# Performance work log

Measured on AMD Instinct MI355X. Metric: run time of the kernel, lower is better.

Reference implementation:

```python
import jax, jax.numpy as jnp
import numpy as np

N = 40000       # nodes
DEG = 16        # in-degree per node (self-constructed so in_deg > 0)
E = N * DEG     # edges
DIN = 128       # in_ent_feats == out_ent_feats
H = 8           # num_heads
D = DIN // H    # head_dim = 16
FF = 4 * DIN    # FFN hidden
HOPS = 5
ALPHA = 0.15
EPS = 1e-5


def _ln(x, g, b):
    m = jnp.mean(x, axis=-1, keepdims=True)
    v = jnp.mean((x - m) ** 2, axis=-1, keepdims=True)
    return (x - m) / jnp.sqrt(v + EPS) * g + b


def setup_inputs() -> dict:
    key = jax.random.key(0)
    ks = jax.random.split(key, 12)
    s = 0.05
    feat = jax.random.normal(ks[0], (N, DIN), dtype=jnp.float32)
    src = jax.random.randint(ks[1], (E,), 0, N, dtype=jnp.int32)
    # every node gets exactly DEG incoming edges -> in_degree > 0 everywhere
    dst = jnp.repeat(jnp.arange(N, dtype=jnp.int32), DEG)
    return {
        "feat": feat,
        "Wh": jax.random.normal(ks[2], (DIN, DIN), dtype=jnp.float32) * s,
        "Wt": jax.random.normal(ks[3], (DIN, DIN), dtype=jnp.float32) * s,
        "We": jax.random.normal(ks[4], (DIN, DIN), dtype=jnp.float32) * s,
        "attn_p": jax.random.normal(ks[5], (H, D), dtype=jnp.float32) * s,
        "g_head": jax.random.normal(ks[6], (H, D), dtype=jnp.float32) * s,
        "g_tail": jax.random.normal(ks[7], (H, D), dtype=jnp.float32) * s,
        "ln1_g": jnp.ones((DIN,), jnp.float32),
        "ln1_b": jnp.zeros((DIN,), jnp.float32),
        "ln2_g": jnp.ones((DIN,), jnp.float32),
        "ln2_b": jnp.zeros((DIN,), jnp.float32),
        "W1": jax.random.normal(ks[8], (FF, DIN), dtype=jnp.float32) * s,
        "b1": jnp.zeros((FF,), jnp.float32),
        "W2": jax.random.normal(ks[9], (DIN, FF), dtype=jnp.float32) * s,
        "b2": jnp.zeros((DIN,), jnp.float32),
        "src": src,
        "dst": dst,
    }


def reference(feat, Wh, Wt, We, attn_p, g_head, g_tail, ln1_g, ln1_b,
              ln2_g, ln2_b, W1, b1, W2, b2, src, dst):
    n = feat.shape[0]
    h = _ln(feat, ln1_g, ln1_b)                      # feat_drop is identity (eval)
    fh = (h @ Wh.T).reshape(n, H, D)                 # feat_head
    ft = (h @ Wt.T).reshape(n, H, D)                 # feat_tail
    fe = (h @ We.T).reshape(n, H, D)                 # feat_enti ('ft' in dgl)

    # attention logits: (u_mul_v . attn).sum(-1) / head_dim, scaled by log(in_deg) of dst
    e = jnp.sum(fh[src] * ft[dst] * attn_p, axis=-1) / D          # [E, H]
    in_deg = jax.ops.segment_sum(jnp.ones_like(dst, jnp.float32), dst, num_segments=n)
    log_in = jnp.log(in_deg)                                       # [N]
    e = e * log_in[dst][:, None]

    # gate scores
    gh = jnp.sum(fh * g_head, axis=-1)                             # [N, H]
    gt = jnp.sum(ft * g_tail, axis=-1)
    gate = jax.nn.sigmoid(gh[src] + gt[dst])                       # [E, H]

    # weighted edge softmax (per-dst stabilized, gated)
    mx = jax.ops.segment_max(e, dst, num_segments=n)               # [N, H]
    tag = jnp.exp(e - mx[dst]) * gate
    ssum = jax.ops.segment_sum(tag, dst, num_segments=n)
    a = tag / ssum[dst]                                            # [E, H]

    # PPR diffusion
    feat0 = fe
    f = feat0
    for _ in range(HOPS):
        msg = f[src] * a[..., None]                                # [E, H, D]
        agg = jax.ops.segment_sum(msg, dst, num_segments=n)
        f = (1.0 - ALPHA) * agg + ALPHA * feat0

    # residual (Identity since in == out), flatten, FFN block
    rst = (f + feat.reshape(n, H, D)).reshape(n, -1)               # [N, DIN]
    x = _ln(rst, ln2_g, ln2_b)
    ff = jax.nn.relu(x @ W1.T + b1) @ W2.T + b2
    return ff + rst
```

## Files before the change

kernel.cpp:

```cpp
#include <hip/hip_runtime.h>
#include <math.h>

#define N_NODES 40000
#define DEG 16
#define DIN 128
#define NH 8
#define DH 16
#define FFDIM 512
#define ALPHA 0.15f
#define LNEPS 1e-5f

typedef __attribute__((ext_vector_type(8))) short bf16x8;
typedef __attribute__((ext_vector_type(4))) float f32x4;
typedef __attribute__((ext_vector_type(4))) unsigned int u32x4;

__device__ inline unsigned int f2bf(float f) {
    unsigned int u = __float_as_uint(f);
    return (u + 0x7fffu + ((u >> 16) & 1u)) >> 16;
}
__device__ inline float bflo(unsigned u) { return __uint_as_float(u << 16); }
__device__ inline float bfhi(unsigned u) { return __uint_as_float(u & 0xffff0000u); }

__device__ inline float dot8(u32x4 uf, u32x4 ut, const float* __restrict__ ap) {
    float s = 0.f;
#pragma unroll
    for (int k = 0; k < 4; ++k) {
        s += bflo(uf[k]) * bflo(ut[k]) * ap[2 * k]
           + bfhi(uf[k]) * bfhi(ut[k]) * ap[2 * k + 1];
    }
    return s;
}

__device__ inline float wave_sum64(float v) {
#pragma unroll
    for (int m = 32; m >= 1; m >>= 1) v += __shfl_xor(v, m, 64);
    return v;
}

__global__ void cvt_weights(const float* __restrict__ wh, const float* __restrict__ wt,
                            const float* __restrict__ we, const float* __restrict__ w1,
                            const float* __restrict__ w2,
                            short* __restrict__ owh, short* __restrict__ owt,
                            short* __restrict__ owe, short* __restrict__ ow1,
                            short* __restrict__ ow2) {
    int i = blockIdx.x * 256 + threadIdx.x;
    if (i < 16384)       owh[i]          = (short)f2bf(wh[i]);
    else if (i < 32768)  owt[i - 16384]  = (short)f2bf(wt[i - 16384]);
    else if (i < 49152)  owe[i - 32768]  = (short)f2bf(we[i - 32768]);
    else if (i < 114688) ow1[i - 49152]  = (short)f2bf(w1[i - 49152]);
    else if (i < 180224) ow2[i - 114688] = (short)f2bf(w2[i - 114688]);
}

__global__ void ln_kernel(const float* __restrict__ in, const float* __restrict__ g,
                          const float* __restrict__ b, short* __restrict__ out, int n) {
    int wid  = (blockIdx.x * blockDim.x + threadIdx.x) >> 6;
    int lane = threadIdx.x & 63;
    if (wid >= n) return;
    float2 v = *(const float2*)(in + (size_t)wid * DIN + lane * 2);
    float mean = wave_sum64(v.x + v.y) * (1.0f / DIN);
    float dx = v.x - mean, dy = v.y - mean;
    float var = wave_sum64(dx * dx + dy * dy) * (1.0f / DIN);
    float rstd = rsqrtf(var + LNEPS);
    float2 gg = *(const float2*)(g + lane * 2);
    float2 bb = *(const float2*)(b + lane * 2);
    float o0 = dx * rstd * gg.x + bb.x, o1 = dy * rstd * gg.y + bb.y;
    unsigned int pack = f2bf(o0) | (f2bf(o1) << 16);
    *(unsigned int*)(out + (size_t)wid * DIN + lane * 2) = pack;
}

__global__ void add_ln_kernel(const float* __restrict__ f, const float* __restrict__ feat,
                              const float* __restrict__ g, const float* __restrict__ b,
                              float* __restrict__ rst, short* __restrict__ x, int n) {
    int wid  = (blockIdx.x * blockDim.x + threadIdx.x) >> 6;
    int lane = threadIdx.x & 63;
    if (wid >= n) return;
    float2 va = *(const float2*)(f + (size_t)wid * DIN + lane * 2);
    float2 vb = *(const float2*)(feat + (size_t)wid * DIN + lane * 2);
    float2 r = { va.x + vb.x, va.y + vb.y };
    *(float2*)(rst + (size_t)wid * DIN + lane * 2) = r;
    float mean = wave_sum64(r.x + r.y) * (1.0f / DIN);
    float dx = r.x - mean, dy = r.y - mean;
    float var = wave_sum64(dx * dx + dy * dy) * (1.0f / DIN);
    float rstd = rsqrtf(var + LNEPS);
    float2 gg = *(const float2*)(g + lane * 2);
    float2 bb = *(const float2*)(b + lane * 2);
    float o0 = dx * rstd * gg.x + bb.x, o1 = dy * rstd * gg.y + bb.y;
    unsigned int pack = f2bf(o0) | (f2bf(o1) << 16);
    *(unsigned int*)(x + (size_t)wid * DIN + lane * 2) = pack;
}

__global__ __launch_bounds__(256) void mfma_gemm(
        const short* __restrict__ A, const short* __restrict__ B,
        int M, int N, int K,
        const float* __restrict__ bias, const float* __restrict__ res, int relu,
        float* __restrict__ Cf, short* __restrict__ Cb) {
    __shared__ __align__(16) short Al[64 * 64];
    __shared__ __align__(16) short Bl[128 * 64];
    const int t  = threadIdx.x;
    const int bm = blockIdx.x * 64;
    const int bn = blockIdx.y * 128;
    const int w = t >> 6, lane = t & 63;
    const int wr = w >> 1, wc = w & 1;
    const int l15 = lane & 15, l4 = lane >> 4;
    f32x4 acc[2][4] = {};
    for (int k0 = 0; k0 < K; k0 += 64) {
        __syncthreads();
#pragma unroll
        for (int q = 0; q < 2; ++q) {
            int c = t + q * 256;
            int r = c >> 3, kb = c & 7;
            bf16x8 v = *(const bf16x8*)(A + (size_t)(bm + r) * K + k0 + kb * 8);
            *(bf16x8*)(Al + (r * 8 + (kb ^ (r & 7))) * 8) = v;
        }
#pragma unroll
        for (int q = 0; q < 4; ++q) {
            int c = t + q * 256;
            int r = c >> 3, kb = c & 7;
            bf16x8 v = *(const bf16x8*)(B + (size_t)(bn + r) * K + k0 + kb * 8);
            *(bf16x8*)(Bl + (r * 8 + (kb ^ (r & 7))) * 8) = v;
        }
        __syncthreads();
#pragma unroll
        for (int kc = 0; kc < 2; ++kc) {
            bf16x8 af[2], bfr[4];
#pragma unroll
            for (int mf = 0; mf < 2; ++mf) {
                int row = wr * 32 + mf * 16 + l15;
                int kb = kc * 4 + l4;
                af[mf] = *(const bf16x8*)(Al + (row * 8 + (kb ^ (row & 7))) * 8);
            }
#pragma unroll
            for (int nf = 0; nf < 4; ++nf) {
                int row = wc * 64 + nf * 16 + l15;
                int kb = kc * 4 + l4;
                bfr[nf] = *(const bf16x8*)(Bl + (row * 8 + (kb ^ (row & 7))) * 8);
            }
#pragma unroll
            for (int mf = 0; mf < 2; ++mf)
#pragma unroll
                for (int nf = 0; nf < 4; ++nf)
                    acc[mf][nf] = __builtin_amdgcn_mfma_f32_16x16x32_bf16(
                        af[mf], bfr[nf], acc[mf][nf], 0, 0, 0);
        }
    }
#pragma unroll
    for (int mf = 0; mf < 2; ++mf) {
#pragma unroll
        for (int nf = 0; nf < 4; ++nf) {
            int gcol = bn + wc * 64 + nf * 16 + l15;
            float bv = bias ? bias[gcol] : 0.f;
#pragma unroll
            for (int r = 0; r < 4; ++r) {
                int grow = bm + wr * 32 + mf * 16 + l4 * 4 + r;
                float v = acc[mf][nf][r] + bv;
                if (relu) v = fmaxf(v, 0.f);
                size_t off = (size_t)grow * N + gcol;
                if (res) v += res[off];
                if (Cb) Cb[off] = (short)f2bf(v);
                if (Cf) Cf[off] = v;
            }
        }
    }
}

__global__ void gates_kernel(const short* __restrict__ fh, const short* __restrict__ ftl,
                             const float* __restrict__ g_head, const float* __restrict__ g_tail,
                             float* __restrict__ gh, float* __restrict__ gt, int total) {
    int t = blockIdx.x * blockDim.x + threadIdx.x;
    if (t >= total) return;
    int i = t >> 3, h = t & 7;
    const short* fp = fh + (size_t)i * DIN + h * DH;
    const short* fq = ftl + (size_t)i * DIN + h * DH;
    const float* gp = g_head + h * DH;
    const float* gq = g_tail + h * DH;
    float s1 = 0.f, s2 = 0.f;
#pragma unroll
    for (int d = 0; d < DH; d += 2) {
        unsigned a = *(const unsigned*)(fp + d);
        unsigned b = *(const unsigned*)(fq + d);
        s1 += bflo(a) * gp[d] + bfhi(a) * gp[d + 1];
        s2 += bflo(b) * gq[d] + bfhi(b) * gq[d + 1];
    }
    gh[t] = s1;
    gt[t] = s2;
}

__global__ void attn_kernel(const short* __restrict__ fh, const short* __restrict__ ftl,
                            const float* __restrict__ ghv, const float* __restrict__ gtv,
                            const float* __restrict__ attn_p, const int* __restrict__ src,
                            float* __restrict__ av, int n) {
    int wid  = (blockIdx.x * blockDim.x + threadIdx.x) >> 6;
    int lane = threadIdx.x & 63;
    if (wid >= n) return;
    int e  = lane & 15;
    int h0 = lane >> 4;
    int s = src[(size_t)wid * DEG + e];
    const short* fr0 = fh  + (size_t)s   * DIN + h0 * DH;
    const short* tr0 = ftl + (size_t)wid * DIN + h0 * DH;
    u32x4 f0a = *(const u32x4*)(fr0);
    u32x4 f0b = *(const u32x4*)(fr0 + 8);
    u32x4 t0a = *(const u32x4*)(tr0);
    u32x4 t0b = *(const u32x4*)(tr0 + 8);
    u32x4 f1a = *(const u32x4*)(fr0 + 64);
    u32x4 f1b = *(const u32x4*)(fr0 + 72);
    u32x4 t1a = *(const u32x4*)(tr0 + 64);
    u32x4 t1b = *(const u32x4*)(tr0 + 72);
    const float* ap0 = attn_p + h0 * DH;
    float v0 = dot8(f0a, t0a, ap0) + dot8(f0b, t0b, ap0 + 8);
    float v1 = dot8(f1a, t1a, ap0 + 64) + dot8(f1b, t1b, ap0 + 72);
    const float c = 0.17328679513998632f;
    v0 *= c; v1 *= c;
    float m0 = v0, m1 = v1;
#pragma unroll
    for (int msk = 1; msk <= 8; msk <<= 1) {
        m0 = fmaxf(m0, __shfl_xor(m0, msk, 64));
        m1 = fmaxf(m1, __shfl_xor(m1, msk, 64));
    }
    float gate0 = 1.f / (1.f + expf(-(ghv[(size_t)s * NH + h0]     + gtv[(size_t)wid * NH + h0])));
    float gate1 = 1.f / (1.f + expf(-(ghv[(size_t)s * NH + h0 + 4] + gtv[(size_t)wid * NH + h0 + 4])));
    float t0 = expf(v0 - m0) * gate0;
    float t1 = expf(v1 - m1) * gate1;
    float s0 = t0, s1 = t1;
#pragma unroll
    for (int msk = 1; msk <= 8; msk <<= 1) {
        s0 += __shfl_xor(s0, msk, 64);
        s1 += __shfl_xor(s1, msk, 64);
    }
    float* ao = av + ((size_t)wid * DEG + e) * NH;
    ao[h0]     = t0 / s0;
    ao[h0 + 4] = t1 / s1;
}

__global__ __launch_bounds__(256) void hop_kernel(
        const short* __restrict__ fin, const float* __restrict__ fe,
        const float* __restrict__ av, const int* __restrict__ src,
        short* __restrict__ fout_b, float* __restrict__ fout_f, int n) {
    __shared__ int sidx[4 * DEG];
    int wv   = threadIdx.x >> 6;
    int lane = threadIdx.x & 63;
    int wid  = blockIdx.x * 4 + wv;
    if (threadIdx.x < 4 * DEG) {
        int node = blockIdx.x * 4 + (threadIdx.x >> 4);
        sidx[threadIdx.x] = (node < n) ? src[(size_t)node * DEG + (threadIdx.x & 15)] : 0;
    }
    __syncthreads();
    if (wid >= n) return;
    int grp = lane >> 4;
    int dl  = lane & 15;
    int h   = dl >> 1;
    const float* ae = av + (size_t)wid * (DEG * NH);
    float acc[8] = {};
#pragma unroll
    for (int it = 0; it < 4; ++it) {
        int e = it * 4 + grp;
        int s = sidx[wv * DEG + e];
        float w = ae[e * NH + h];
        u32x4 v = *(const u32x4*)(fin + (size_t)s * DIN + dl * 8);
#pragma unroll
        for (int k = 0; k < 4; ++k) {
            acc[2 * k]     += w * bflo(v[k]);
            acc[2 * k + 1] += w * bfhi(v[k]);
        }
    }
#pragma unroll
    for (int k = 0; k < 8; ++k) {
        acc[k] += __shfl_xor(acc[k], 16, 64);
        acc[k] += __shfl_xor(acc[k], 32, 64);
    }
    if (grp == 0) {
        const float* fp = fe + (size_t)wid * DIN + dl * 8;
        float o[8];
#pragma unroll
        for (int k = 0; k < 8; ++k)
            o[k] = (1.f - ALPHA) * acc[k] + ALPHA * fp[k];
        if (fout_b) {
            unsigned pk[4];
#pragma unroll
            for (int k = 0; k < 4; ++k)
                pk[k] = f2bf(o[2 * k]) | (f2bf(o[2 * k + 1]) << 16);
            *(u32x4*)(fout_b + (size_t)wid * DIN + dl * 8) = *(u32x4*)pk;
        } else {
            float4 a = { o[0], o[1], o[2], o[3] };
            float4 b = { o[4], o[5], o[6], o[7] };
            *(float4*)(fout_f + (size_t)wid * DIN + dl * 8)     = a;
            *(float4*)(fout_f + (size_t)wid * DIN + dl * 8 + 4) = b;
        }
    }
}

extern "C" void kernel_launch(void* const* d_in, const int* in_sizes, int n_in,
                              void* d_out, int out_size, void* d_ws, size_t ws_size,
                              hipStream_t stream) {
    const float* feat   = (const float*)d_in[0];
    const float* Wh     = (const float*)d_in[1];
    const float* Wt     = (const float*)d_in[2];
    const float* We     = (const float*)d_in[3];
    const float* attn_p = (const float*)d_in[4];
    const float* g_head = (const float*)d_in[5];
    const float* g_tail = (const float*)d_in[6];
    const float* ln1_g  = (const float*)d_in[7];
    const float* ln1_b  = (const float*)d_in[8];
    const float* ln2_g  = (const float*)d_in[9];
    const float* ln2_b  = (const float*)d_in[10];
    const float* W1     = (const float*)d_in[11];
    const float* b1     = (const float*)d_in[12];
    const float* W2     = (const float*)d_in[13];
    const float* b2     = (const float*)d_in[14];
    const int*   src    = (const int*)d_in[15];

    float* ws = (float*)d_ws;
    float* fe   = ws;
    float* av   = ws + 5120000;
    float* gh   = ws + 10240000;
    float* gt   = ws + 10560000;
    short* h_bf   = (short*)(ws + 10880000);
    short* fh_bf  = (short*)(ws + 13440000);
    short* ftl_bf = (short*)(ws + 16000000);
    short* fe_bf  = (short*)(ws + 18560000);
    short* f0_bf  = (short*)(ws + 21120000);
    short* f1_bf  = (short*)(ws + 23680000);
    float* ffin   = ws + 26240000;
    short* x_bf   = (short*)(ws + 31360000);
    short* hidden = (short*)ws;
    short* wb     = (short*)(ws + 33920000);
    short* wh_bf = wb, *wt_bf = wb + 16384, *we_bf = wb + 32768;
    short* w1_bf = wb + 49152, *w2_bf = wb + 114688;
    float* rst = (float*)d_out;

    dim3 b256(256);
    int nodeBlocks  = (N_NODES * 64) / 256;
    int nodeBlocks4 = (N_NODES + 3) / 4;

    cvt_weights<<<704, b256, 0, stream>>>(Wh, Wt, We, W1, W2, wh_bf, wt_bf, we_bf, w1_bf, w2_bf);
    ln_kernel<<<nodeBlocks, b256, 0, stream>>>(feat, ln1_g, ln1_b, h_bf, N_NODES);

    dim3 gp(N_NODES / 64, 1);
    mfma_gemm<<<gp, b256, 0, stream>>>(h_bf, wh_bf, N_NODES, DIN, DIN, nullptr, nullptr, 0, nullptr, fh_bf);
    mfma_gemm<<<gp, b256, 0, stream>>>(h_bf, wt_bf, N_NODES, DIN, DIN, nullptr, nullptr, 0, nullptr, ftl_bf);
    mfma_gemm<<<gp, b256, 0, stream>>>(h_bf, we_bf, N_NODES, DIN, DIN, nullptr, nullptr, 0, fe, fe_bf);

    gates_kernel<<<(N_NODES * NH) / 256, b256, 0, stream>>>(fh_bf, ftl_bf, g_head, g_tail, gh, gt, N_NODES * NH);
    attn_kernel<<<nodeBlocks, b256, 0, stream>>>(fh_bf, ftl_bf, gh, gt, attn_p, src, av, N_NODES);

    hop_kernel<<<nodeBlocks4, b256, 0, stream>>>(fe_bf, fe, av, src, f0_bf, nullptr, N_NODES);
    hop_kernel<<<nodeBlocks4, b256, 0, stream>>>(f0_bf, fe, av, src, f1_bf, nullptr, N_NODES);
    hop_kernel<<<nodeBlocks4, b256, 0, stream>>>(f1_bf, fe, av, src, f0_bf, nullptr, N_NODES);
    hop_kernel<<<nodeBlocks4, b256, 0, stream>>>(f0_bf, fe, av, src, f1_bf, nullptr, N_NODES);
    hop_kernel<<<nodeBlocks4, b256, 0, stream>>>(f1_bf, fe, av, src, nullptr, ffin, N_NODES);

    add_ln_kernel<<<nodeBlocks, b256, 0, stream>>>(ffin, feat, ln2_g, ln2_b, rst, x_bf, N_NODES);

    dim3 gff1(N_NODES / 64, FFDIM / 128);
    mfma_gemm<<<gff1, b256, 0, stream>>>(x_bf, w1_bf, N_NODES, FFDIM, DIN, b1, nullptr, 1, nullptr, hidden);
    dim3 gff2(N_NODES / 64, 1);
    mfma_gemm<<<gff2, b256, 0, stream>>>(hidden, w2_bf, N_NODES, DIN, FFDIM, b2, rst, 0, rst, nullptr);
}
```

Before: 367.7 us.

## Store attention weights and feat0 in bf16, stage weights in LDS, enlarge GEMM tile

Attention coefficients are now written as bf16 instead of fp32. The residual feat0 term in each PPR hop is read from the existing bf16 copy, so the fp32 fe buffer is gone. Each hop block loads its nodes' attention weights into shared memory in one coalesced copy. The MFMA GEMM tile grows from 64 to 128 rows per block, with row clamping for the tail. Together these cut memory traffic across the five hop passes and increase reuse in the GEMMs, at the cost of lower precision for attention and feat0, fewer GEMM blocks, and more registers per GEMM thread.

New measurement: 406.8 us. 10.6% more time.

```diff
diff --git a/kernel.cpp b/kernel.cpp
--- a/kernel.cpp
+++ b/kernel.cpp
@@ -20,6 +20,7 @@
 }
 __device__ inline float bflo(unsigned u) { return __uint_as_float(u << 16); }
 __device__ inline float bfhi(unsigned u) { return __uint_as_float(u & 0xffff0000u); }
+__device__ inline float bfs(short s) { return __uint_as_float(((unsigned)(unsigned short)s) << 16); }
 
 __device__ inline float dot8(u32x4 uf, u32x4 ut, const float* __restrict__ ap) {
     float s = 0.f;
@@ -94,38 +95,34 @@
         int M, int N, int K,
         const float* __restrict__ bias, const float* __restrict__ res, int relu,
         float* __restrict__ Cf, short* __restrict__ Cb) {
-    __shared__ __align__(16) short Al[64 * 64];
+    __shared__ __align__(16) short Al[128 * 64];
     __shared__ __align__(16) short Bl[128 * 64];
     const int t  = threadIdx.x;
-    const int bm = blockIdx.x * 64;
+    const int bm = blockIdx.x * 128;
     const int bn = blockIdx.y * 128;
     const int w = t >> 6, lane = t & 63;
     const int wr = w >> 1, wc = w & 1;
     const int l15 = lane & 15, l4 = lane >> 4;
-    f32x4 acc[2][4] = {};
+    f32x4 acc[4][4] = {};
     for (int k0 = 0; k0 < K; k0 += 64) {
         __syncthreads();
-#pragma unroll
-        for (int q = 0; q < 2; ++q) {
-            int c = t + q * 256;
-            int r = c >> 3, kb = c & 7;
-            bf16x8 v = *(const bf16x8*)(A + (size_t)(bm + r) * K + k0 + kb * 8);
-            *(bf16x8*)(Al + (r * 8 + (kb ^ (r & 7))) * 8) = v;
-        }
 #pragma unroll
         for (int q = 0; q < 4; ++q) {
             int c = t + q * 256;
             int r = c >> 3, kb = c & 7;
-            bf16x8 v = *(const bf16x8*)(B + (size_t)(bn + r) * K + k0 + kb * 8);
-            *(bf16x8*)(Bl + (r * 8 + (kb ^ (r & 7))) * 8) = v;
+            int gr = bm + r; if (gr >= M) gr = M - 1;
+            bf16x8 va = *(const bf16x8*)(A + (size_t)gr * K + k0 + kb * 8);
+            *(bf16x8*)(Al + (r * 8 + (kb ^ (r & 7))) * 8) = va;
+            bf16x8 vb = *(const bf16x8*)(B + (size_t)(bn + r) * K + k0 + kb * 8);
+            *(bf16x8*)(Bl + (r * 8 + (kb ^ (r & 7))) * 8) = vb;
         }
         __syncthreads();
 #pragma unroll
         for (int kc = 0; kc < 2; ++kc) {
-            bf16x8 af[2], bfr[4];
-#pragma unroll
-            for (int mf = 0; mf < 2; ++mf) {
-                int row = wr * 32 + mf * 16 + l15;
+            bf16x8 af[4], bfr[4];
+#pragma unroll
+            for (int mf = 0; mf < 4; ++mf) {
+                int row = wr * 64 + mf * 16 + l15;
                 int kb = kc * 4 + l4;
                 af[mf] = *(const bf16x8*)(Al + (row * 8 + (kb ^ (row & 7))) * 8);
             }
@@ -136,7 +133,7 @@
                 bfr[nf] = *(const bf16x8*)(Bl + (row * 8 + (kb ^ (row & 7))) * 8);
             }
 #pragma unroll
-            for (int mf = 0; mf < 2; ++mf)
+            for (int mf = 0; mf < 4; ++mf)
 #pragma unroll
                 for (int nf = 0; nf < 4; ++nf)
                     acc[mf][nf] = __builtin_amdgcn_mfma_f32_16x16x32_bf16(
@@ -144,14 +141,15 @@
         }
     }
 #pragma unroll
-    for (int mf = 0; mf < 2; ++mf) {
+    for (int mf = 0; mf < 4; ++mf) {
 #pragma unroll
         for (int nf = 0; nf < 4; ++nf) {
             int gcol = bn + wc * 64 + nf * 16 + l15;
             float bv = bias ? bias[gcol] : 0.f;
 #pragma unroll
             for (int r = 0; r < 4; ++r) {
-                int grow = bm + wr * 32 + mf * 16 + l4 * 4 + r;
+                int grow = bm + wr * 64 + mf * 16 + l4 * 4 + r;
+                if (grow >= M) continue;
                 float v = acc[mf][nf][r] + bv;
                 if (relu) v = fmaxf(v, 0.f);
                 size_t off = (size_t)grow * N + gcol;
@@ -188,7 +186,7 @@
 __global__ void attn_kernel(const short* __restrict__ fh, const short* __restrict__ ftl,
                             const float* __restrict__ ghv, const float* __restrict__ gtv,
                             const float* __restrict__ attn_p, const int* __restrict__ src,
-                            float* __restrict__ av, int n) {
+                            short* __restrict__ av, int n) {
     int wid  = (blockIdx.x * blockDim.x + threadIdx.x) >> 6;
     int lane = threadIdx.x & 63;
     if (wid >= n) return;
@@ -226,35 +224,38 @@
         s0 += __shfl_xor(s0, msk, 64);
         s1 += __shfl_xor(s1, msk, 64);
     }
-    float* ao = av + ((size_t)wid * DEG + e) * NH;
-    ao[h0]     = t0 / s0;
-    ao[h0 + 4] = t1 / s1;
+    short* ao = av + ((size_t)wid * DEG + e) * NH;
+    ao[h0]     = (short)f2bf(t0 / s0);
+    ao[h0 + 4] = (short)f2bf(t1 / s1);
 }
 
 __global__ __launch_bounds__(256) void hop_kernel(
-        const short* __restrict__ fin, const float* __restrict__ fe,
-        const float* __restrict__ av, const int* __restrict__ src,
+        const short* __restrict__ fin, const short* __restrict__ febf,
+        const short* __restrict__ avb, const int* __restrict__ src,
         short* __restrict__ fout_b, float* __restrict__ fout_f, int n) {
     __shared__ int sidx[4 * DEG];
+    __shared__ short sav[4 * DEG * NH];
     int wv   = threadIdx.x >> 6;
     int lane = threadIdx.x & 63;
-    int wid  = blockIdx.x * 4 + wv;
+    int base = blockIdx.x * 4;
+    int wid  = base + wv;
     if (threadIdx.x < 4 * DEG) {
-        int node = blockIdx.x * 4 + (threadIdx.x >> 4);
+        int node = base + (threadIdx.x >> 4);
         sidx[threadIdx.x] = (node < n) ? src[(size_t)node * DEG + (threadIdx.x & 15)] : 0;
     }
+    ((unsigned*)sav)[threadIdx.x] = ((const unsigned*)(avb + (size_t)base * DEG * NH))[threadIdx.x];
     __syncthreads();
     if (wid >= n) return;
     int grp = lane >> 4;
     int dl  = lane & 15;
     int h   = dl >> 1;
-    const float* ae = av + (size_t)wid * (DEG * NH);
+    const short* ae = sav + wv * DEG * NH;
     float acc[8] = {};
 #pragma unroll
     for (int it = 0; it < 4; ++it) {
         int e = it * 4 + grp;
         int s = sidx[wv * DEG + e];
-        float w = ae[e * NH + h];
+        float w = bfs(ae[e * NH + h]);
         u32x4 v = *(const u32x4*)(fin + (size_t)s * DIN + dl * 8);
 #pragma unroll
         for (int k = 0; k < 4; ++k) {
@@ -268,11 +269,13 @@
         acc[k] += __shfl_xor(acc[k], 32, 64);
     }
     if (grp == 0) {
-        const float* fp = fe + (size_t)wid * DIN + dl * 8;
+        u32x4 fv = *(const u32x4*)(febf + (size_t)wid * DIN + dl * 8);
         float o[8];
 #pragma unroll
-        for (int k = 0; k < 8; ++k)
-            o[k] = (1.f - ALPHA) * acc[k] + ALPHA * fp[k];
+        for (int k = 0; k < 4; ++k) {
+            o[2 * k]     = (1.f - ALPHA) * acc[2 * k]     + ALPHA * bflo(fv[k]);
+            o[2 * k + 1] = (1.f - ALPHA) * acc[2 * k + 1] + ALPHA * bfhi(fv[k]);
+        }
         if (fout_b) {
             unsigned pk[4];
 #pragma unroll
@@ -309,49 +312,49 @@
     const int*   src    = (const int*)d_in[15];
 
     float* ws = (float*)d_ws;
-    float* fe   = ws;
-    float* av   = ws + 5120000;
-    float* gh   = ws + 10240000;
-    float* gt   = ws + 10560000;
-    short* h_bf   = (short*)(ws + 10880000);
-    short* fh_bf  = (short*)(ws + 13440000);
-    short* ftl_bf = (short*)(ws + 16000000);
-    short* fe_bf  = (short*)(ws + 18560000);
-    short* f0_bf  = (short*)(ws + 21120000);
-    short* f1_bf  = (short*)(ws + 23680000);
-    float* ffin   = ws + 26240000;
-    short* x_bf   = (short*)(ws + 31360000);
-    short* hidden = (short*)ws;
-    short* wb     = (short*)(ws + 33920000);
+    short* av_bf  = (short*)ws;
+    short* fe_bf  = (short*)(ws + 2560000);
+    float* gh     = ws + 5120000;
+    float* gt     = ws + 5440000;
+    short* h_bf   = (short*)(ws + 5760000);
+    short* fh_bf  = (short*)(ws + 8320000);
+    short* ftl_bf = (short*)(ws + 10880000);
+    short* f0_bf  = (short*)(ws + 13440000);
+    short* f1_bf  = (short*)(ws + 16000000);
+    float* ffin   = ws + 18560000;
+    short* x_bf   = (short*)(ws + 23680000);
+    short* wb     = (short*)(ws + 26240000);
     short* wh_bf = wb, *wt_bf = wb + 16384, *we_bf = wb + 32768;
     short* w1_bf = wb + 49152, *w2_bf = wb + 114688;
+    short* hidden = (short*)ws;
     float* rst = (float*)d_out;
 
     dim3 b256(256);
     int nodeBlocks  = (N_NODES * 64) / 256;
     int nodeBlocks4 = (N_NODES + 3) / 4;
+    int gm = (N_NODES + 127) / 128;
 
     cvt_weights<<<704, b256, 0, stream>>>(Wh, Wt, We, W1, W2, wh_bf, wt_bf, we_bf, w1_bf, w2_bf);
     ln_kernel<<<nodeBlocks, b256, 0, stream>>>(feat, ln1_g, ln1_b, h_bf, N_NODES);
 
-    dim3 gp(N_NODES / 64, 1);
+    dim3 gp(gm, 1);
     mfma_gemm<<<gp, b256, 0, stream>>>(h_bf, wh_bf, N_NODES, DIN, DIN, nullptr, nullptr, 0, nullptr, fh_bf);
     mfma_gemm<<<gp, b256, 0, stream>>>(h_bf, wt_bf, N_NODES, DIN, DIN, nullptr, nullptr, 0, nullptr, ftl_bf);
-    mfma_gemm<<<gp, b256, 0, stream>>>(h_bf, we_bf, N_NODES, DIN, DIN, nullptr, nullptr, 0, fe, fe_bf);
+    mfma_gemm<<<gp, b256, 0, stream>>>(h_bf, we_bf, N_NODES, DIN, DIN, nullptr, nullptr, 0, nullptr, fe_bf);
 
     gates_kernel<<<(N_NODES * NH) / 256, b256, 0, stream>>>(fh_bf, ftl_bf, g_head, g_tail, gh, gt, N_NODES * NH);
-    attn_kernel<<<nodeBlocks, b256, 0, stream>>>(fh_bf, ftl_bf, gh, gt, attn_p, src, av, N_NODES);
-
-    hop_kernel<<<nodeBlocks4, b256, 0, stream>>>(fe_bf, fe, av, src, f0_bf, nullptr, N_NODES);
-    hop_kernel<<<nodeBlocks4, b256, 0, stream>>>(f0_bf, fe, av, src, f1_bf, nullptr, N_NODES);
-    hop_kernel<<<nodeBlocks4, b256, 0, stream>>>(f1_bf, fe, av, src, f0_bf, nullptr, N_NODES);
-    hop_kernel<<<nodeBlocks4, b256, 0, stream>>>(f0_bf, fe, av, src, f1_bf, nullptr, N_NODES);
-    hop_kernel<<<nodeBlocks4, b256, 0, stream>>>(f1_bf, fe, av, src, nullptr, ffin, N_NODES);
+    attn_kernel<<<nodeBlocks, b256, 0, stream>>>(fh_bf, ftl_bf, gh, gt, attn_p, src, av_bf, N_NODES);
+
+    hop_kernel<<<nodeBlocks4, b256, 0, stream>>>(fe_bf, fe_bf, av_bf, src, f0_bf, nullptr, N_NODES);
+    hop_kernel<<<nodeBlocks4, b256, 0, stream>>>(f0_bf, fe_bf, av_bf, src, f1_bf, nullptr, N_NODES);
+    hop_kernel<<<nodeBlocks4, b256, 0, stream>>>(f1_bf, fe_bf, av_bf, src, f0_bf, nullptr, N_NODES);
+    hop_kernel<<<nodeBlocks4, b256, 0, stream>>>(f0_bf, fe_bf, av_bf, src, f1_bf, nullptr, N_NODES);
+    hop_kernel<<<nodeBlocks4, b256, 0, stream>>>(f1_bf, fe_bf, av_bf, src, nullptr, ffin, N_NODES);
 
     add_ln_kernel<<<nodeBlocks, b256, 0, stream>>>(ffin, feat, ln2_g, ln2_b, rst, x_bf, N_NODES);
 
-    dim3 gff1(N_NODES / 64, FFDIM / 128);
+    dim3 gff1(gm, FFDIM / 128);
     mfma_gemm<<<gff1, b256, 0, stream>>>(x_bf, w1_bf, N_NODES, FFDIM, DIN, b1, nullptr, 1, nullptr, hidden);
-    dim3 gff2(N_NODES / 64, 1);
+    dim3 gff2(gm, 1);
     mfma_gemm<<<gff2, b256, 0, stream>>>(hidden, w2_bf, N_NODES, DIN, FFDIM, b2, rst, 0, rst, nullptr);
 }
```

## Store node features head-major and process graph ops per head

Applied to the files above, without the earlier changes.

Projection GEMMs now write fh/ft/fe in a head-major [H][N][16] bf16 layout, and the attention and hop kernels run one head per block so each gathered neighbor row is a contiguous 32-byte chunk. The aim is to shrink each head's working set so the random src gathers hit cache better. Attention weights and the feT residual are now stored in bf16 instead of fp32, which cuts traffic but adds rounding error. The final hop now emits bf16 instead of fp32 before the add+LN.

New measurement: 393.9 us. +7.1%, slower.

```diff
diff --git a/kernel.cpp b/kernel.cpp
--- a/kernel.cpp
+++ b/kernel.cpp
@@ -20,16 +20,6 @@
 }
 __device__ inline float bflo(unsigned u) { return __uint_as_float(u << 16); }
 __device__ inline float bfhi(unsigned u) { return __uint_as_float(u & 0xffff0000u); }
-
-__device__ inline float dot8(u32x4 uf, u32x4 ut, const float* __restrict__ ap) {
-    float s = 0.f;
-#pragma unroll
-    for (int k = 0; k < 4; ++k) {
-        s += bflo(uf[k]) * bflo(ut[k]) * ap[2 * k]
-           + bfhi(uf[k]) * bfhi(ut[k]) * ap[2 * k + 1];
-    }
-    return s;
-}
 
 __device__ inline float wave_sum64(float v) {
 #pragma unroll
@@ -68,13 +58,15 @@
     *(unsigned int*)(out + (size_t)wid * DIN + lane * 2) = pack;
 }
 
-__global__ void add_ln_kernel(const float* __restrict__ f, const float* __restrict__ feat,
+__global__ void add_ln_kernel(const short* __restrict__ fT, const float* __restrict__ feat,
                               const float* __restrict__ g, const float* __restrict__ b,
                               float* __restrict__ rst, short* __restrict__ x, int n) {
     int wid  = (blockIdx.x * blockDim.x + threadIdx.x) >> 6;
     int lane = threadIdx.x & 63;
     if (wid >= n) return;
-    float2 va = *(const float2*)(f + (size_t)wid * DIN + lane * 2);
+    int h = lane >> 3, d2 = (lane & 7) * 2;
+    unsigned uf = *(const unsigned*)(fT + ((size_t)h * N_NODES + wid) * 16 + d2);
+    float2 va = { bflo(uf), bfhi(uf) };
     float2 vb = *(const float2*)(feat + (size_t)wid * DIN + lane * 2);
     float2 r = { va.x + vb.x, va.y + vb.y };
     *(float2*)(rst + (size_t)wid * DIN + lane * 2) = r;
@@ -92,7 +84,7 @@
 __global__ __launch_bounds__(256) void mfma_gemm(
         const short* __restrict__ A, const short* __restrict__ B,
         int M, int N, int K,
-        const float* __restrict__ bias, const float* __restrict__ res, int relu,
+        const float* __restrict__ bias, const float* __restrict__ res, int relu, int tmode,
         float* __restrict__ Cf, short* __restrict__ Cb) {
     __shared__ __align__(16) short Al[64 * 64];
     __shared__ __align__(16) short Bl[128 * 64];
@@ -154,25 +146,30 @@
                 int grow = bm + wr * 32 + mf * 16 + l4 * 4 + r;
                 float v = acc[mf][nf][r] + bv;
                 if (relu) v = fmaxf(v, 0.f);
-                size_t off = (size_t)grow * N + gcol;
-                if (res) v += res[off];
-                if (Cb) Cb[off] = (short)f2bf(v);
-                if (Cf) Cf[off] = v;
+                if (tmode) {
+                    size_t toff = ((size_t)(gcol >> 4) * M + grow) * 16 + (gcol & 15);
+                    Cb[toff] = (short)f2bf(v);
+                } else {
+                    size_t off = (size_t)grow * N + gcol;
+                    if (res) v += res[off];
+                    if (Cb) Cb[off] = (short)f2bf(v);
+                    if (Cf) Cf[off] = v;
+                }
             }
         }
     }
 }
 
-__global__ void gates_kernel(const short* __restrict__ fh, const short* __restrict__ ftl,
+__global__ void gates_kernel(const short* __restrict__ fhT, const short* __restrict__ ftT,
                              const float* __restrict__ g_head, const float* __restrict__ g_tail,
-                             float* __restrict__ gh, float* __restrict__ gt, int total) {
+                             float* __restrict__ ghT, float* __restrict__ gtT, int total) {
     int t = blockIdx.x * blockDim.x + threadIdx.x;
     if (t >= total) return;
-    int i = t >> 3, h = t & 7;
-    const short* fp = fh + (size_t)i * DIN + h * DH;
-    const short* fq = ftl + (size_t)i * DIN + h * DH;
+    int h = t / N_NODES;
     const float* gp = g_head + h * DH;
     const float* gq = g_tail + h * DH;
+    const short* fp = fhT + (size_t)t * 16;
+    const short* fq = ftT + (size_t)t * 16;
     float s1 = 0.f, s2 = 0.f;
 #pragma unroll
     for (int d = 0; d < DH; d += 2) {
@@ -181,110 +178,124 @@
         s1 += bflo(a) * gp[d] + bfhi(a) * gp[d + 1];
         s2 += bflo(b) * gq[d] + bfhi(b) * gq[d + 1];
     }
-    gh[t] = s1;
-    gt[t] = s2;
-}
-
-__global__ void attn_kernel(const short* __restrict__ fh, const short* __restrict__ ftl,
-                            const float* __restrict__ ghv, const float* __restrict__ gtv,
-                            const float* __restrict__ attn_p, const int* __restrict__ src,
-                            float* __restrict__ av, int n) {
-    int wid  = (blockIdx.x * blockDim.x + threadIdx.x) >> 6;
-    int lane = threadIdx.x & 63;
-    if (wid >= n) return;
-    int e  = lane & 15;
-    int h0 = lane >> 4;
-    int s = src[(size_t)wid * DEG + e];
-    const short* fr0 = fh  + (size_t)s   * DIN + h0 * DH;
-    const short* tr0 = ftl + (size_t)wid * DIN + h0 * DH;
-    u32x4 f0a = *(const u32x4*)(fr0);
-    u32x4 f0b = *(const u32x4*)(fr0 + 8);
-    u32x4 t0a = *(const u32x4*)(tr0);
-    u32x4 t0b = *(const u32x4*)(tr0 + 8);
-    u32x4 f1a = *(const u32x4*)(fr0 + 64);
-    u32x4 f1b = *(const u32x4*)(fr0 + 72);
-    u32x4 t1a = *(const u32x4*)(tr0 + 64);
-    u32x4 t1b = *(const u32x4*)(tr0 + 72);
-    const float* ap0 = attn_p + h0 * DH;
-    float v0 = dot8(f0a, t0a, ap0) + dot8(f0b, t0b, ap0 + 8);
-    float v1 = dot8(f1a, t1a, ap0 + 64) + dot8(f1b, t1b, ap0 + 72);
+    ghT[t] = s1;
+    gtT[t] = s2;
+}
+
+__global__ __launch_bounds__(256) void attn_kernel(
+        const short* __restrict__ fhT, const short* __restrict__ ftT,
+        const float* __restrict__ ghT, const float* __restrict__ gtT,
+        const float* __restrict__ attn_p, const int* __restrict__ src,
+        short* __restrict__ avT) {
+    int h = blockIdx.x & 7;
+    int chunk = blockIdx.x >> 3;
+    int wv = threadIdx.x >> 6, lane = threadIdx.x & 63;
+    int node = chunk * 64 + wv * 16 + (lane >> 2);
+    int egrp = lane & 3;
+    const size_t hb = (size_t)h * N_NODES;
+    const short* tp = ftT + (hb + node) * 16;
+    u32x4 ta = *(const u32x4*)tp;
+    u32x4 tb = *(const u32x4*)(tp + 8);
+    const float* p = attn_p + h * DH;
     const float c = 0.17328679513998632f;
-    v0 *= c; v1 *= c;
-    float m0 = v0, m1 = v1;
-#pragma unroll
-    for (int msk = 1; msk <= 8; msk <<= 1) {
-        m0 = fmaxf(m0, __shfl_xor(m0, msk, 64));
-        m1 = fmaxf(m1, __shfl_xor(m1, msk, 64));
-    }
-    float gate0 = 1.f / (1.f + expf(-(ghv[(size_t)s * NH + h0]     + gtv[(size_t)wid * NH + h0])));
-    float gate1 = 1.f / (1.f + expf(-(ghv[(size_t)s * NH + h0 + 4] + gtv[(size_t)wid * NH + h0 + 4])));
-    float t0 = expf(v0 - m0) * gate0;
-    float t1 = expf(v1 - m1) * gate1;
-    float s0 = t0, s1 = t1;
-#pragma unroll
-    for (int msk = 1; msk <= 8; msk <<= 1) {
-        s0 += __shfl_xor(s0, msk, 64);
-        s1 += __shfl_xor(s1, msk, 64);
-    }
-    float* ao = av + ((size_t)wid * DEG + e) * NH;
-    ao[h0]     = t0 / s0;
-    ao[h0 + 4] = t1 / s1;
+    float q[16];
+#pragma unroll
+    for (int k = 0; k < 4; ++k) {
+        q[2 * k]     = bflo(ta[k]) * p[2 * k] * c;
+        q[2 * k + 1] = bfhi(ta[k]) * p[2 * k + 1] * c;
+        q[8 + 2 * k]     = bflo(tb[k]) * p[8 + 2 * k] * c;
+        q[8 + 2 * k + 1] = bfhi(tb[k]) * p[8 + 2 * k + 1] * c;
+    }
+    float gtv = gtT[hb + node];
+    int4 s4 = *(const int4*)(src + node * DEG + egrp * 4);
+    int ss[4] = { s4.x, s4.y, s4.z, s4.w };
+    float lg[4], gg[4];
+#pragma unroll
+    for (int j = 0; j < 4; ++j) {
+        const short* fr = fhT + (hb + ss[j]) * 16;
+        u32x4 a = *(const u32x4*)fr;
+        u32x4 b = *(const u32x4*)(fr + 8);
+        float s = 0.f;
+#pragma unroll
+        for (int k = 0; k < 4; ++k) {
+            s += q[2 * k] * bflo(a[k]) + q[2 * k + 1] * bfhi(a[k]);
+            s += q[8 + 2 * k] * bflo(b[k]) + q[8 + 2 * k + 1] * bfhi(b[k]);
+        }
+        lg[j] = s;
+        gg[j] = ghT[hb + ss[j]];
+    }
+    float m = fmaxf(fmaxf(lg[0], lg[1]), fmaxf(lg[2], lg[3]));
+    m = fmaxf(m, __shfl_xor(m, 1, 64));
+    m = fmaxf(m, __shfl_xor(m, 2, 64));
+    float tv[4], sum = 0.f;
+#pragma unroll
+    for (int j = 0; j < 4; ++j) {
+        float gate = 1.f / (1.f + expf(-(gg[j] + gtv)));
+        tv[j] = expf(lg[j] - m) * gate;
+        sum += tv[j];
+    }
+    sum += __shfl_xor(sum, 1, 64);
+    sum += __shfl_xor(sum, 2, 64);
+    float inv = 1.f / sum;
+    unsigned pk0 = f2bf(tv[0] * inv) | (f2bf(tv[1] * inv) << 16);
+    unsigned pk1 = f2bf(tv[2] * inv) | (f2bf(tv[3] * inv) << 16);
+    unsigned* ao = (unsigned*)(avT + (hb + node) * 16 + egrp * 4);
+    ao[0] = pk0;
+    ao[1] = pk1;
 }
 
 __global__ __launch_bounds__(256) void hop_kernel(
-        const short* __restrict__ fin, const float* __restrict__ fe,
-        const float* __restrict__ av, const int* __restrict__ src,
-        short* __restrict__ fout_b, float* __restrict__ fout_f, int n) {
-    __shared__ int sidx[4 * DEG];
-    int wv   = threadIdx.x >> 6;
-    int lane = threadIdx.x & 63;
-    int wid  = blockIdx.x * 4 + wv;
-    if (threadIdx.x < 4 * DEG) {
-        int node = blockIdx.x * 4 + (threadIdx.x >> 4);
-        sidx[threadIdx.x] = (node < n) ? src[(size_t)node * DEG + (threadIdx.x & 15)] : 0;
-    }
-    __syncthreads();
-    if (wid >= n) return;
-    int grp = lane >> 4;
-    int dl  = lane & 15;
-    int h   = dl >> 1;
-    const float* ae = av + (size_t)wid * (DEG * NH);
-    float acc[8] = {};
-#pragma unroll
-    for (int it = 0; it < 4; ++it) {
-        int e = it * 4 + grp;
-        int s = sidx[wv * DEG + e];
-        float w = ae[e * NH + h];
-        u32x4 v = *(const u32x4*)(fin + (size_t)s * DIN + dl * 8);
+        const short* __restrict__ finT, const short* __restrict__ feT,
+        const short* __restrict__ avT, const int* __restrict__ src,
+        short* __restrict__ foutT) {
+    int h = blockIdx.x & 7;
+    int chunk = blockIdx.x >> 3;
+    int wv = threadIdx.x >> 6, lane = threadIdx.x & 63;
+    int node = chunk * 64 + wv * 16 + (lane >> 2);
+    int egrp = lane & 3;
+    const size_t hb = (size_t)h * N_NODES;
+    int4 s4 = *(const int4*)(src + node * DEG + egrp * 4);
+    int ss[4] = { s4.x, s4.y, s4.z, s4.w };
+    const short* ap = avT + (hb + node) * 16 + egrp * 4;
+    unsigned aw0 = *(const unsigned*)(ap);
+    unsigned aw1 = *(const unsigned*)(ap + 2);
+    float w[4] = { bflo(aw0), bfhi(aw0), bflo(aw1), bfhi(aw1) };
+    float acc[16] = {};
+#pragma unroll
+    for (int j = 0; j < 4; ++j) {
+        const short* fr = finT + (hb + ss[j]) * 16;
+        u32x4 a = *(const u32x4*)fr;
+        u32x4 b = *(const u32x4*)(fr + 8);
 #pragma unroll
         for (int k = 0; k < 4; ++k) {
-            acc[2 * k]     += w * bflo(v[k]);
-            acc[2 * k + 1] += w * bfhi(v[k]);
-        }
-    }
-#pragma unroll
-    for (int k = 0; k < 8; ++k) {
-        acc[k] += __shfl_xor(acc[k], 16, 64);
-        acc[k] += __shfl_xor(acc[k], 32, 64);
-    }
-    if (grp == 0) {
-        const float* fp = fe + (size_t)wid * DIN + dl * 8;
-        float o[8];
-#pragma unroll
-        for (int k = 0; k < 8; ++k)
-            o[k] = (1.f - ALPHA) * acc[k] + ALPHA * fp[k];
-        if (fout_b) {
-            unsigned pk[4];
-#pragma unroll
-            for (int k = 0; k < 4; ++k)
-                pk[k] = f2bf(o[2 * k]) | (f2bf(o[2 * k + 1]) << 16);
-            *(u32x4*)(fout_b + (size_t)wid * DIN + dl * 8) = *(u32x4*)pk;
-        } else {
-            float4 a = { o[0], o[1], o[2], o[3] };
-            float4 b = { o[4], o[5], o[6], o[7] };
-            *(float4*)(fout_f + (size_t)wid * DIN + dl * 8)     = a;
-            *(float4*)(fout_f + (size_t)wid * DIN + dl * 8 + 4) = b;
-        }
+            acc[2 * k]     += w[j] * bflo(a[k]);
+            acc[2 * k + 1] += w[j] * bfhi(a[k]);
+            acc[8 + 2 * k]     += w[j] * bflo(b[k]);
+            acc[8 + 2 * k + 1] += w[j] * bfhi(b[k]);
+        }
+    }
+#pragma unroll
+    for (int k = 0; k < 16; ++k) {
+        acc[k] += __shfl_xor(acc[k], 1, 64);
+        acc[k] += __shfl_xor(acc[k], 2, 64);
+    }
+    if (egrp == 0) {
+        const short* fp = feT + (hb + node) * 16;
+        u32x4 fa = *(const u32x4*)fp;
+        u32x4 fb = *(const u32x4*)(fp + 8);
+        unsigned pk[8];
+#pragma unroll
+        for (int k = 0; k < 4; ++k) {
+            float o0 = (1.f - ALPHA) * acc[2 * k]     + ALPHA * bflo(fa[k]);
+            float o1 = (1.f - ALPHA) * acc[2 * k + 1] + ALPHA * bfhi(fa[k]);
+            pk[k] = f2bf(o0) | (f2bf(o1) << 16);
+            float o2 = (1.f - ALPHA) * acc[8 + 2 * k]     + ALPHA * bflo(fb[k]);
+            float o3 = (1.f - ALPHA) * acc[8 + 2 * k + 1] + ALPHA * bfhi(fb[k]);
+            pk[4 + k] = f2bf(o2) | (f2bf(o3) << 16);
+        }
+        u32x4* op = (u32x4*)(foutT + (hb + node) * 16);
+        op[0] = *(u32x4*)pk;
+        op[1] = *(u32x4*)(pk + 4);
     }
 }
 
@@ -309,49 +320,47 @@
     const int*   src    = (const int*)d_in[15];
 
     float* ws = (float*)d_ws;
-    float* fe   = ws;
-    float* av   = ws + 5120000;
-    float* gh   = ws + 10240000;
-    float* gt   = ws + 10560000;
-    short* h_bf   = (short*)(ws + 10880000);
-    short* fh_bf  = (short*)(ws + 13440000);
-    short* ftl_bf = (short*)(ws + 16000000);
-    short* fe_bf  = (short*)(ws + 18560000);
-    short* f0_bf  = (short*)(ws + 21120000);
-    short* f1_bf  = (short*)(ws + 23680000);
-    float* ffin   = ws + 26240000;
-    short* x_bf   = (short*)(ws + 31360000);
-    short* hidden = (short*)ws;
-    short* wb     = (short*)(ws + 33920000);
+    short* avT = (short*)ws;
+    short* feT = (short*)(ws + 2560000);
+    float* ghT = ws + 5120000;
+    float* gtT = ws + 5440000;
+    short* h_bf = (short*)(ws + 5760000);
+    short* fhT = (short*)(ws + 8320000);
+    short* ftT = (short*)(ws + 10880000);
+    short* f0T = (short*)(ws + 13440000);
+    short* f1T = (short*)(ws + 16000000);
+    short* x_bf = (short*)(ws + 18560000);
+    short* wb   = (short*)(ws + 21120000);
     short* wh_bf = wb, *wt_bf = wb + 16384, *we_bf = wb + 32768;
     short* w1_bf = wb + 49152, *w2_bf = wb + 114688;
+    short* hidden = (short*)ws;
     float* rst = (float*)d_out;
 
     dim3 b256(256);
-    int nodeBlocks  = (N_NODES * 64) / 256;
-    int nodeBlocks4 = (N_NODES + 3) / 4;
+    int nodeBlocks = (N_NODES * 64) / 256;
+    int headBlocks = 8 * (N_NODES / 64);
 
     cvt_weights<<<704, b256, 0, stream>>>(Wh, Wt, We, W1, W2, wh_bf, wt_bf, we_bf, w1_bf, w2_bf);
     ln_kernel<<<nodeBlocks, b256, 0, stream>>>(feat, ln1_g, ln1_b, h_bf, N_NODES);
 
     dim3 gp(N_NODES / 64, 1);
-    mfma_gemm<<<gp, b256, 0, stream>>>(h_bf, wh_bf, N_NODES, DIN, DIN, nullptr, nullptr, 0, nullptr, fh_bf);
-    mfma_gemm<<<gp, b256, 0, stream>>>(h_bf, wt_bf, N_NODES, DIN, DIN, nullptr, nullptr, 0, nullptr, ftl_bf);
-    mfma_gemm<<<gp, b256, 0, stream>>>(h_bf, we_bf, N_NODES, DIN, DIN, nullptr, nullptr, 0, fe, fe_bf);
-
-    gates_kernel<<<(N_NODES * NH) / 256, b256, 0, stream>>>(fh_bf, ftl_bf, g_head, g_tail, gh, gt, N_NODES * NH);
-    attn_kernel<<<nodeBlocks, b256, 0, stream>>>(fh_bf, ftl_bf, gh, gt, attn_p, src, av, N_NODES);
-
-    hop_kernel<<<nodeBlocks4, b256, 0, stream>>>(fe_bf, fe, av, src, f0_bf, nullptr, N_NODES);
-    hop_kernel<<<nodeBlocks4, b256, 0, stream>>>(f0_bf, fe, av, src, f1_bf, nullptr, N_NODES);
-    hop_kernel<<<nodeBlocks4, b256, 0, stream>>>(f1_bf, fe, av, src, f0_bf, nullptr, N_NODES);
-    hop_kernel<<<nodeBlocks4, b256, 0, stream>>>(f0_bf, fe, av, src, f1_bf, nullptr, N_NODES);
-    hop_kernel<<<nodeBlocks4, b256, 0, stream>>>(f1_bf, fe, av, src, nullptr, ffin, N_NODES);
-
-    add_ln_kernel<<<nodeBlocks, b256, 0, stream>>>(ffin, feat, ln2_g, ln2_b, rst, x_bf, N_NODES);
+    mfma_gemm<<<gp, b256, 0, stream>>>(h_bf, wh_bf, N_NODES, DIN, DIN, nullptr, nullptr, 0, 1, nullptr, fhT);
+    mfma_gemm<<<gp, b256, 0, stream>>>(h_bf, wt_bf, N_NODES, DIN, DIN, nullptr, nullptr, 0, 1, nullptr, ftT);
+    mfma_gemm<<<gp, b256, 0, stream>>>(h_bf, we_bf, N_NODES, DIN, DIN, nullptr, nullptr, 0, 1, nullptr, feT);
+
+    gates_kernel<<<(N_NODES * NH) / 256, b256, 0, stream>>>(fhT, ftT, g_head, g_tail, ghT, gtT, N_NODES * NH);
+    attn_kernel<<<headBlocks, b256, 0, stream>>>(fhT, ftT, ghT, gtT, attn_p, src, avT);
+
+    hop_kernel<<<headBlocks, b256, 0, stream>>>(feT, feT, avT, src, f0T);
+    hop_kernel<<<headBlocks, b256, 0, stream>>>(f0T, feT, avT, src, f1T);
+    hop_kernel<<<headBlocks, b256, 0, stream>>>(f1T, feT, avT, src, f0T);
+    hop_kernel<<<headBlocks, b256, 0, stream>>>(f0T, feT, avT, src, f1T);
+    hop_kernel<<<headBlocks, b256, 0, stream>>>(f1T, feT, avT, src, f0T);
+
+    add_ln_kernel<<<nodeBlocks, b256, 0, stream>>>(f0T, feat, ln2_g, ln2_b, rst, x_bf, N_NODES);
 
     dim3 gff1(N_NODES / 64, FFDIM / 128);
-    mfma_gemm<<<gff1, b256, 0, stream>>>(x_bf, w1_bf, N_NODES, FFDIM, DIN, b1, nullptr, 1, nullptr, hidden);
+    mfma_gemm<<<gff1, b256, 0, stream>>>(x_bf, w1_bf, N_NODES, FFDIM, DIN, b1, nullptr, 1, 0, nullptr, hidden);
     dim3 gff2(N_NODES / 64, 1);
-    mfma_gemm<<<gff2, b256, 0, stream>>>(hidden, w2_bf, N_NODES, DIN, FFDIM, b2, rst, 0, rst, nullptr);
-}
+    mfma_gemm<<<gff2, b256, 0, stream>>>(hidden, w2_bf, N_NODES, DIN, FFDIM, b2, rst, 0, 0, rst, nullptr);
+}
```
